# Kernel tuning notes

Measured on AMD Instinct MI355X. Metric: run time of the kernel, lower is better.

## Reference

```python
import jax, jax.numpy as jnp
import numpy as np

CAP = 15.0
EPS = 1e-6
NUM_HEADS = 16
HEAD_DIM = 64

def _rmsnorm(x, w):
    xf = x.astype(jnp.float32)
    var = jnp.mean(xf * xf, axis=-1, keepdims=True)
    return w * (xf * jax.lax.rsqrt(var + EPS)).astype(x.dtype)

def _gate(g):
    # sigmoid(soft_cap(g)) with cap 15
    return jax.nn.sigmoid(CAP * jnp.tanh(g / CAP))

def setup_inputs() -> dict:
    key = jax.random.key(0)
    ks = jax.random.split(key, 4)
    B, S, D = 4, 2048, 1024
    H, Dh = NUM_HEADS, HEAD_DIM
    return {
        "x": jax.random.normal(ks[0], (B, S, D), jnp.float32),
        "hidden_state": jnp.zeros((B, H, Dh, Dh), jnp.float32),
        "w_rms": jnp.ones((D,), jnp.float32),
        "w_qkv": jax.random.normal(ks[1], (D, 3 * H * Dh), jnp.float32) * 0.02,
        "w_gate": jax.random.normal(ks[2], (D, 3 * H), jnp.float32) * 0.02,
        "w_out": jax.random.normal(ks[3], (D, D), jnp.float32) * 0.02,
    }

def reference(x, hidden_state, w_rms, w_qkv, w_gate, w_out):
    B, S, D = x.shape
    H, Dh = NUM_HEADS, HEAD_DIM
    residual = x
    xn = _rmsnorm(x, w_rms)
    qkv = (xn @ w_qkv).reshape(B, S, 3, H, Dh)
    q, k, v = qkv[:, :, 0], qkv[:, :, 1], qkv[:, :, 2]  # [B,S,H,Dh]
    gates = _gate((xn @ w_gate).reshape(B, S, 3, H))
    i_g, f_g, o_g = gates[:, :, 0], gates[:, :, 1], gates[:, :, 2]  # [B,S,H]

    # time-major for scan: [S,B,H,...]
    def tm(a):
        return jnp.moveaxis(a, 1, 0)

    def step(state, inp):
        qt, kt, vt, it, ft, ot = inp  # [B,H,Dh]/[B,H]
        kv = kt[..., :, None] * vt[..., None, :]            # [B,H,Dh,Dh]
        state = ft[..., None, None] * state + it[..., None, None] * kv
        h = jnp.einsum('bhd,bhde->bhe', qt, state) * ot[..., None]
        return state, h

    _, h_seq = jax.lax.scan(step, hidden_state,
                            (tm(q), tm(k), tm(v), tm(i_g), tm(f_g), tm(o_g)))
    out = jnp.moveaxis(h_seq, 0, 1).reshape(B, S, H * Dh) @ w_out
    return residual + out
```

## Files before the change

kernel.cpp:

```cpp
#include <hip/hip_runtime.h>
#include <math.h>

typedef unsigned short u16;
typedef unsigned int   u32;
typedef __bf16 bf16x8 __attribute__((ext_vector_type(8)));
typedef float  f32x4  __attribute__((ext_vector_type(4)));

#define NBATCH 4
#define SEQ    2048
#define DIM    1024
#define NH     16
#define BH     64
#define NC     32
#define ROWS   8192
#define N1     3328

__device__ __forceinline__ u16 f2bf(float f) {
  u32 u = __builtin_bit_cast(u32, f);
  u32 r = u + 0x7fffu + ((u >> 16) & 1u);
  return (u16)(r >> 16);
}
__device__ __forceinline__ float bf2f(u16 h) {
  return __builtin_bit_cast(float, (u32)h << 16);
}

__device__ __forceinline__ void gl2lds16(const u16* g, u16* l) {
  __builtin_amdgcn_global_load_lds(
      (const __attribute__((address_space(1))) u32*)g,
      (__attribute__((address_space(3))) u32*)l, 16, 0, 0);
}

__global__ __launch_bounds__(256) void transpose_w(const float* __restrict__ W,
                                                   u16* __restrict__ Bt, int K, int N) {
  __shared__ float tile[32][33];
  const int n0 = blockIdx.x * 32, k0 = blockIdx.y * 32;
  const int tx = threadIdx.x, ty = threadIdx.y;
  #pragma unroll
  for (int i = 0; i < 4; i++)
    tile[ty + i * 8][tx] = W[(size_t)(k0 + ty + i * 8) * N + n0 + tx];
  __syncthreads();
  #pragma unroll
  for (int i = 0; i < 4; i++)
    Bt[(size_t)(n0 + ty + i * 8) * K + k0 + tx] = f2bf(tile[tx][ty + i * 8]);
}

__global__ __launch_bounds__(256) void fill_gateW(const float* __restrict__ wg,
                                                  u16* __restrict__ Bt) {
  const int g = blockIdx.x;
  const int tid = threadIdx.x;
  #pragma unroll
  for (int kk = 0; kk < 4; kk++) {
    const int k = kk * 256 + tid;
    u16 v = 0;
    if (g < 48) v = f2bf(wg[(size_t)k * 48 + g]);
    Bt[(size_t)(3072 + g) * 1024 + k] = v;
  }
}

__global__ __launch_bounds__(256) void rmsnorm_k(const float* __restrict__ x,
                                                 const float* __restrict__ w,
                                                 u16* __restrict__ xn) {
  const int row = blockIdx.x, tid = threadIdx.x;
  const float4 xv = *(const float4*)&x[(size_t)row * 1024 + tid * 4];
  float ss = xv.x * xv.x + xv.y * xv.y + xv.z * xv.z + xv.w * xv.w;
  #pragma unroll
  for (int off = 32; off > 0; off >>= 1) ss += __shfl_down(ss, off);
  __shared__ float red[4];
  if ((tid & 63) == 0) red[tid >> 6] = ss;
  __syncthreads();
  const float tot = red[0] + red[1] + red[2] + red[3];
  const float scale = rsqrtf(tot * (1.0f / 1024.0f) + 1e-6f);
  const float4 wv = *(const float4*)&w[tid * 4];
  const u16 o0 = f2bf(xv.x * scale * wv.x), o1 = f2bf(xv.y * scale * wv.y);
  const u16 o2 = f2bf(xv.z * scale * wv.z), o3 = f2bf(xv.w * scale * wv.w);
  uint2 ov;
  ov.x = (u32)o0 | ((u32)o1 << 16);
  ov.y = (u32)o2 | ((u32)o3 << 16);
  *(uint2*)&xn[(size_t)row * 1024 + tid * 4] = ov;
}


#define FENCE asm volatile("" ::: "memory")
#define SBAR  do { FENCE; __builtin_amdgcn_s_barrier(); FENCE; } while (0)
#define WAITV4 do { FENCE; asm volatile("s_waitcnt vmcnt(4)" ::: "memory"); } while (0)
#define WAITV0 do { FENCE; asm volatile("s_waitcnt vmcnt(0)" ::: "memory"); } while (0)

#define STAGE_A(BUF, HALF, TILE) do { \
  const u16* s_ = Abase + (size_t)(TILE) * 64 + (size_t)(HALF) * 131072; \
  u16* l_ = &lds[((BUF) * 4 + (HALF)) * 8192 + tid * 8]; \
  gl2lds16(s_, l_); gl2lds16(s_ + 65536, l_ + 4096); \
} while (0)

#define STAGE_B(BUF, HALF, TILE) do { \
  const u16* s_ = Bbase + (size_t)(TILE) * 64 + (size_t)(HALF) * 131072; \
  u16* l_ = &lds[((BUF) * 4 + 2 + (HALF)) * 8192 + tid * 8]; \
  gl2lds16(s_, l_); gl2lds16(s_ + 65536, l_ + 4096); \
} while (0)

#define READ_A(ALDS, MH) do { \
  _Pragma("unroll") \
  for (int mi_ = 0; mi_ < 4; ++mi_) { \
    af[mi_][0] = *(const bf16x8*)((ALDS) + (MH) * 4096 + mi_ * 1024 + co0); \
    af[mi_][1] = *(const bf16x8*)((ALDS) + (MH) * 4096 + mi_ * 1024 + co1); \
  } \
} while (0)

#define READ_B(BLDS, NH) do { \
  _Pragma("unroll") \
  for (int ni_ = 0; ni_ < 2; ++ni_) { \
    bfr[NH][ni_][0] = *(const bf16x8*)((BLDS) + (NH) * 2048 + ni_ * 1024 + co0); \
    bfr[NH][ni_][1] = *(const bf16x8*)((BLDS) + (NH) * 2048 + ni_ * 1024 + co1); \
  } \
} while (0)

#define MFMA16(MH, NH) do { \
  __builtin_amdgcn_s_setprio(1); \
  _Pragma("unroll") \
  for (int mi_ = 0; mi_ < 4; ++mi_) { \
    _Pragma("unroll") \
    for (int ni_ = 0; ni_ < 2; ++ni_) { \
      acc[(MH)*4+mi_][(NH)*2+ni_] = __builtin_amdgcn_mfma_f32_16x16x32_bf16( \
          af[mi_][0], bfr[NH][ni_][0], acc[(MH)*4+mi_][(NH)*2+ni_], 0, 0, 0); \
      acc[(MH)*4+mi_][(NH)*2+ni_] = __builtin_amdgcn_mfma_f32_16x16x32_bf16( \
          af[mi_][1], bfr[NH][ni_][1], acc[(MH)*4+mi_][(NH)*2+ni_], 0, 0, 0); \
    } \
  } \
  __builtin_amdgcn_s_setprio(0); \
} while (0)

#define GITER(T, FULL) do { \
   READ_A(aLds0, 0); READ_B(bLds0, 0); STAGE_A(1, 0, 2*(T)+1); \
         SBAR; MFMA16(0, 0); SBAR; \
   READ_B(bLds0, 1); STAGE_A(1, 1, 2*(T)+1); \
         SBAR; MFMA16(0, 1); SBAR; \
   READ_A(aLds0, 1); if (FULL) STAGE_B(0, 0, 2*(T)+2); \
         SBAR; MFMA16(1, 0); SBAR; \
   if (FULL) STAGE_B(0, 1, 2*(T)+2); \
         SBAR; MFMA16(1, 1); if (FULL) { WAITV4; } else { WAITV0; } SBAR; \
   READ_A(aLds1, 0); READ_B(bLds1, 0); if (FULL) STAGE_A(0, 0, 2*(T)+2); \
         SBAR; MFMA16(0, 0); SBAR; \
   READ_B(bLds1, 1); if (FULL) STAGE_A(0, 1, 2*(T)+2); \
         SBAR; MFMA16(0, 1); SBAR; \
   READ_A(aLds1, 1); if (FULL) STAGE_B(1, 0, 2*(T)+3); \
         SBAR; MFMA16(1, 0); SBAR; \
   if (FULL) STAGE_B(1, 1, 2*(T)+3); \
         SBAR; MFMA16(1, 1); if (FULL) { WAITV4; } SBAR; \
} while (0)

__global__ __launch_bounds__(512, 2) void gemm_qkv(const u16* __restrict__ A, const u16* __restrict__ Bt,
                                                   u16* __restrict__ Qb, u16* __restrict__ Kb,
                                                   u16* __restrict__ Vb, float* __restrict__ gates) {
  __shared__ __attribute__((aligned(16))) u16 lds[65536];
  const int tid = threadIdx.x;
  const int lane = tid & 63, wave = tid >> 6;
  const int q = lane >> 4, m16 = lane & 15;
  const int wm = wave & 1, wn = wave >> 1;

  const int g = blockIdx.x;
  const int swz = (g & 7) * 52 + (g >> 3);
  const int bm = swz & 31, bn = swz >> 5;
  const int rowBase = bm * 256, colBase = bn * 256;

  const int sx = m16 & 7;
  const int co0 = (q ^ sx) * 8;
  const int co1 = ((4 + q) ^ sx) * 8;

  const int r0 = tid >> 3, pc = tid & 7;
  const int lcg = pc ^ (r0 & 7);
  const u16* Abase = A  + (size_t)rowBase * 1024 + (size_t)r0 * 1024 + lcg * 8;
  const u16* Bbase = Bt + (size_t)colBase * 1024 + (size_t)r0 * 1024 + lcg * 8;

  const u16* aLds0 = &lds[wm * 8192 + m16 * 64];
  const u16* aLds1 = aLds0 + 32768;
  const u16* bLds0 = &lds[16384 + (wn >> 1) * 8192 + ((wn & 1) * 64 + m16) * 64];
  const u16* bLds1 = bLds0 + 32768;

  bf16x8 af[4][2];
  bf16x8 bfr[2][2][2];
  f32x4 acc[8][4] = {};

  STAGE_A(0, 0, 0); STAGE_A(0, 1, 0); STAGE_B(0, 0, 0); STAGE_B(0, 1, 0);
  STAGE_B(1, 0, 1); STAGE_B(1, 1, 1);
  WAITV4; SBAR;

  #pragma unroll 1
  for (int t = 0; t < 7; ++t) GITER(t, 1);
  GITER(7, 0);

  const int rr = lane >> 2, co = (lane & 3) * 16;
  if (colBase < 3072) {
    const int which = colBase >> 10;
    u16* dstBase = (which == 0) ? Qb : ((which == 1) ? Kb : Vb);
    const int b = rowBase >> 11;
    const int h = ((colBase & 1023) >> 6) + wn;
    const int tRow0 = (rowBase & 2047) + wm * 128;
    u16* headBase = dstBase + ((size_t)(b * 16 + h)) * 2048 * 64;
    u16* scratch = lds + wave * 1024;
    #pragma unroll
    for (int mi = 0; mi < 8; ++mi) {
      #pragma unroll
      for (int bj = 0; bj < 4; ++bj)
        #pragma unroll
        for (int r = 0; r < 4; ++r)
          scratch[(q * 4 + r) * 64 + bj * 16 + m16] = f2bf(acc[mi][bj][r]);
      const uint4 d0 = *(const uint4*)&scratch[rr * 64 + co];
      const uint4 d1 = *(const uint4*)&scratch[rr * 64 + co + 8];
      u16* gp = headBase + (size_t)(tRow0 + mi * 16 + rr) * 64 + co;
      *(uint4*)gp = d0;
      *(uint4*)(gp + 8) = d1;
    }
  } else {
    if (wn == 0) {
      #pragma unroll
      for (int ai = 0; ai < 8; ++ai)
        #pragma unroll
        for (int bj = 0; bj < 3; ++bj)
          #pragma unroll
          for (int r = 0; r < 4; ++r) {
            const int grow = rowBase + wm * 128 + ai * 16 + q * 4 + r;
            const int b = grow >> 11, tt = grow & 2047;
            const float v = acc[ai][bj][r];
            const float gg = 1.0f / (1.0f + expf(-(15.0f * tanhf(v * (1.0f / 15.0f)))));
            gates[((size_t)bj * 64 + (b * 16 + m16)) * 2048 + tt] = gg;
          }
    }
  }
}

__device__ __forceinline__ void gemm_core128(const u16* __restrict__ A, const u16* __restrict__ Bt,
                                             int K, int rowBase, int colBase,
                                             u16* As, u16* Bs, f32x4 (&acc)[4][4]) {
  const int tid = threadIdx.x;
  const int lane = tid & 63;
  const int q = lane >> 4, m16 = lane & 15;
  const int wave = tid >> 6;
  const int wm = wave & 1, wn = wave >> 1;
  const u16* gA[4]; u16* lA[4];
  const u16* gB[4]; u16* lB[4];
  #pragma unroll
  for (int j = 0; j < 4; j++) {
    const int c = tid + j * 256;
    const int half = c >> 9, cc = c & 511;
    gA[j] = &A [(size_t)(rowBase + (cc >> 2)) * K + half * 32 + (cc & 3) * 8];
    lA[j] = As + c * 8;
    gB[j] = &Bt[(size_t)(colBase + (cc >> 2)) * K + half * 32 + (cc & 3) * 8];
    lB[j] = Bs + c * 8;
  }
  for (int kb = 0; kb < K / 64; ++kb) {
    __syncthreads();
    #pragma unroll
    for (int j = 0; j < 4; j++) { gl2lds16(gA[j], lA[j]); gA[j] += 64; }
    #pragma unroll
    for (int j = 0; j < 4; j++) { gl2lds16(gB[j], lB[j]); gB[j] += 64; }
    __syncthreads();
    #pragma unroll
    for (int ks = 0; ks < 2; ks++) {
      const int off = ks * 4096;
      bf16x8 af[4], bfr[4];
      #pragma unroll
      for (int mi = 0; mi < 4; mi++)
        af[mi] = *(const bf16x8*)&As[off + (wm * 64 + mi * 16 + m16) * 32 + q * 8];
      #pragma unroll
      for (int ni = 0; ni < 4; ni++)
        bfr[ni] = *(const bf16x8*)&Bs[off + (wn * 64 + ni * 16 + m16) * 32 + q * 8];
      #pragma unroll
      for (int mi = 0; mi < 4; mi++)
        #pragma unroll
        for (int ni = 0; ni < 4; ni++)
          acc[mi][ni] = __builtin_amdgcn_mfma_f32_16x16x32_bf16(af[mi], bfr[ni], acc[mi][ni], 0, 0, 0);
    }
  }
}

__global__ __launch_bounds__(256, 4) void gemm_out(const u16* __restrict__ A, const u16* __restrict__ Bt,
                                                   const float* __restrict__ resid,
                                                   float* __restrict__ out) {
  __shared__ __attribute__((aligned(16))) u16 As[128 * 64];
  __shared__ __attribute__((aligned(16))) u16 Bs[128 * 64];
  f32x4 acc[4][4] = {};
  const int rowBase = blockIdx.x * 128, colBase = blockIdx.y * 128;
  gemm_core128(A, Bt, 1024, rowBase, colBase, As, Bs, acc);
  const int tid = threadIdx.x;
  const int lane = tid & 63, wave = tid >> 6;
  const int q = lane >> 4, m16 = lane & 15;
  const int wm = wave & 1, wn = wave >> 1;
  #pragma unroll
  for (int mi = 0; mi < 4; mi++)
    #pragma unroll
    for (int ni = 0; ni < 4; ni++)
      #pragma unroll
      for (int r = 0; r < 4; r++) {
        const int grow = rowBase + wm * 64 + mi * 16 + q * 4 + r;
        const int gcol = colBase + wn * 64 + ni * 16 + m16;
        const size_t idx = (size_t)grow * 1024 + gcol;
        out[idx] = acc[mi][ni][r] + resid[idx];
      }
}

__global__ __launch_bounds__(256) void passA_k(const u16* __restrict__ Qb, const u16* __restrict__ Kb,
                                               const u16* __restrict__ Vb,
                                               const float* __restrict__ gates,
                                               float* __restrict__ la,
                                               u16* __restrict__ Mbuf, u16* __restrict__ hseq) {
  __shared__ u16 Ql[64][72], Kl[64][72], KTl[64][72], VTl[64][72], Pl[64][72];
  __shared__ float laS[64], iS[64];
  const int tid = threadIdx.x;
  const int bh = blockIdx.x >> 5, c = blockIdx.x & 31;
  const int lane = tid & 63, w = tid >> 6;
  const int q = lane >> 4, m16 = lane & 15;
  const size_t base = ((size_t)bh * 2048 + c * 64) * 64;
  const int toff = c * 64;

  if (tid < 64) {
    float lg = logf(gates[(size_t)(64 + bh) * 2048 + toff + tid]);
    #pragma unroll
    for (int off = 1; off < 64; off <<= 1) {
      const float y = __shfl_up(lg, off);
      if (tid >= off) lg += y;
    }
    laS[tid] = lg;
    iS[tid] = gates[(size_t)bh * 2048 + toff + tid];
    la[(size_t)bh * 2048 + toff + tid] = lg;
  }
  __syncthreads();

  {
    const int s = tid >> 2, db = (tid & 3) * 16;
    const float wk = expf(laS[63] - laS[s]) * iS[s];
    const uint4 q0 = *(const uint4*)&Qb[base + s * 64 + db];
    const uint4 q1 = *(const uint4*)&Qb[base + s * 64 + db + 8];
    *(uint4*)&Ql[s][db] = q0;
    *(uint4*)&Ql[s][db + 8] = q1;
    const uint4 k0 = *(const uint4*)&Kb[base + s * 64 + db];
    const uint4 k1 = *(const uint4*)&Kb[base + s * 64 + db + 8];
    *(uint4*)&Kl[s][db] = k0;
    *(uint4*)&Kl[s][db + 8] = k1;
    u16 ktmp[16];
    *(uint4*)&ktmp[0] = k0;
    *(uint4*)&ktmp[8] = k1;
    #pragma unroll
    for (int j = 0; j < 16; j++) KTl[db + j][s] = f2bf(wk * bf2f(ktmp[j]));
    const uint4 v0 = *(const uint4*)&Vb[base + s * 64 + db];
    const uint4 v1 = *(const uint4*)&Vb[base + s * 64 + db + 8];
    u16 vtmp[16];
    *(uint4*)&vtmp[0] = v0;
    *(uint4*)&vtmp[8] = v1;
    #pragma unroll
    for (int j = 0; j < 16; j++) VTl[db + j][s] = vtmp[j];
  }
  __syncthreads();

  f32x4 pacc[4] = {};
  #pragma unroll
  for (int ks = 0; ks < 2; ks++) {
    const bf16x8 aq = *(const bf16x8*)&Ql[w * 16 + m16][ks * 32 + q * 8];
    #pragma unroll
    for (int ni = 0; ni < 4; ni++) {
      const bf16x8 bk = *(const bf16x8*)&Kl[ni * 16 + m16][ks * 32 + q * 8];
      pacc[ni] = __builtin_amdgcn_mfma_f32_16x16x32_bf16(aq, bk, pacc[ni], 0, 0, 0);
    }
  }
  #pragma unroll
  for (int ni = 0; ni < 4; ni++)
    #pragma unroll
    for (int r = 0; r < 4; r++) {
      const int tt = w * 16 + q * 4 + r, ss = ni * 16 + m16;
      float Wts = 0.0f;
      if (ss <= tt) Wts = expf(laS[tt] - laS[ss]) * iS[ss];
      Pl[tt][ss] = f2bf(pacc[ni][r] * Wts);
    }
  __syncthreads();

  f32x4 hacc[4] = {}, macc[4] = {};
  #pragma unroll
  for (int ks = 0; ks < 2; ks++) {
    const bf16x8 ap = *(const bf16x8*)&Pl[w * 16 + m16][ks * 32 + q * 8];
    const bf16x8 av = *(const bf16x8*)&VTl[w * 16 + m16][ks * 32 + q * 8];
    #pragma unroll
    for (int ni = 0; ni < 4; ni++) {
      const bf16x8 bv = *(const bf16x8*)&VTl[ni * 16 + m16][ks * 32 + q * 8];
      const bf16x8 bk = *(const bf16x8*)&KTl[ni * 16 + m16][ks * 32 + q * 8];
      hacc[ni] = __builtin_amdgcn_mfma_f32_16x16x32_bf16(ap, bv, hacc[ni], 0, 0, 0);
      macc[ni] = __builtin_amdgcn_mfma_f32_16x16x32_bf16(av, bk, macc[ni], 0, 0, 0);
    }
  }
  const int b = bh >> 4, h = bh & 15;
  #pragma unroll
  for (int ni = 0; ni < 4; ni++)
    #pragma unroll
    for (int r = 0; r < 4; r++) {
      const int tt = w * 16 + q * 4 + r, e = ni * 16 + m16;
      const int tg = c * 64 + tt;
      hseq[((size_t)b * 2048 + tg) * 1024 + h * 64 + e] = f2bf(hacc[ni][r]);
      Mbuf[(((size_t)bh * 32 + c) * 64 + tt) * 64 + e] = f2bf(macc[ni][r]);
    }
}

__global__ __launch_bounds__(256) void passB_k(u16* __restrict__ Mbuf,
                                               const float* __restrict__ hidden,
                                               const float* __restrict__ la) {
  const int bh = blockIdx.x >> 4;
  const int e = (blockIdx.x & 15) * 256 + threadIdx.x;
  __shared__ float Gs[32];
  if (threadIdx.x < 32)
    Gs[threadIdx.x] = expf(la[(size_t)bh * 2048 + threadIdx.x * 64 + 63]);
  __syncthreads();
  const int eRow = e >> 6, dCol = e & 63;
  float st = hidden[(size_t)bh * 4096 + dCol * 64 + eRow];
  u16* M = &Mbuf[(size_t)bh * 32 * 4096 + e];
  float m_next = bf2f(M[0]);
  #pragma unroll 4
  for (int c = 0; c < 32; c++) {
    const float m_cur = m_next;
    if (c < 31) m_next = bf2f(M[(size_t)(c + 1) * 4096]);
    M[(size_t)c * 4096] = f2bf(st);
    st = Gs[c] * st + m_cur;
  }
}

__global__ __launch_bounds__(256) void passC_k(const u16* __restrict__ Qb,
                                               const u16* __restrict__ SprevT,
                                               const float* __restrict__ la,
                                               const float* __restrict__ gates,
                                               u16* __restrict__ hseq) {
  __shared__ u16 aQl[64][72], STl[64][72];
  __shared__ float laS[64], oS[64];
  const int tid = threadIdx.x;
  const int bh = blockIdx.x >> 5, c = blockIdx.x & 31;
  const int lane = tid & 63, w = tid >> 6;
  const int q = lane >> 4, m16 = lane & 15;
  const size_t base = ((size_t)bh * 2048 + c * 64) * 64;
  const int toff = c * 64;
  if (tid < 64) {
    laS[tid] = la[(size_t)bh * 2048 + toff + tid];
    oS[tid] = gates[(size_t)(128 + bh) * 2048 + toff + tid];
  }
  {
    const int s = tid >> 2, db = (tid & 3) * 16;
    *(uint4*)&aQl[s][db]     = *(const uint4*)&Qb[base + s * 64 + db];
    *(uint4*)&aQl[s][db + 8] = *(const uint4*)&Qb[base + s * 64 + db + 8];
    const u16* SpT = &SprevT[((size_t)bh * 32 + c) * 4096];
    *(uint4*)&STl[s][db]     = *(const uint4*)&SpT[s * 64 + db];
    *(uint4*)&STl[s][db + 8] = *(const uint4*)&SpT[s * 64 + db + 8];
  }
  __syncthreads();
  f32x4 acc[4] = {};
  #pragma unroll
  for (int ks = 0; ks < 2; ks++) {
    const bf16x8 a = *(const bf16x8*)&aQl[w * 16 + m16][ks * 32 + q * 8];
    #pragma unroll
    for (int ni = 0; ni < 4; ni++) {
      const bf16x8 bb = *(const bf16x8*)&STl[ni * 16 + m16][ks * 32 + q * 8];
      acc[ni] = __builtin_amdgcn_mfma_f32_16x16x32_bf16(a, bb, acc[ni], 0, 0, 0);
    }
  }
  const int b = bh >> 4, h = bh & 15;
  #pragma unroll
  for (int ni = 0; ni < 4; ni++)
    #pragma unroll
    for (int r = 0; r < 4; r++) {
      const int tt = w * 16 + q * 4 + r, e = ni * 16 + m16;
      const int tg = c * 64 + tt;
      const float a_t = expf(laS[tt]);
      const float o = oS[tt];
      const size_t idx = ((size_t)b * 2048 + tg) * 1024 + h * 64 + e;
      hseq[idx] = f2bf(o * (bf2f(hseq[idx]) + a_t * acc[ni][r]));
    }
}

extern "C" void kernel_launch(void* const* d_in, const int* in_sizes, int n_in,
                              void* d_out, int out_size, void* d_ws, size_t ws_size,
                              hipStream_t stream) {
  (void)in_sizes; (void)n_in; (void)out_size; (void)ws_size;
  const float* x      = (const float*)d_in[0];
  const float* hidden = (const float*)d_in[1];
  const float* w_rms  = (const float*)d_in[2];
  const float* w_qkv  = (const float*)d_in[3];
  const float* w_gate = (const float*)d_in[4];
  const float* w_out  = (const float*)d_in[5];
  float* out = (float*)d_out;

  char* p = (char*)d_ws;
  u16* wqkvT = (u16*)p;  p += (size_t)N1 * 1024 * 2;
  u16* woutT = (u16*)p;  p += (size_t)1024 * 1024 * 2;
  u16* xn    = (u16*)p;  p += (size_t)ROWS * 1024 * 2;
  u16* Qb    = (u16*)p;  p += (size_t)BH * 2048 * 64 * 2;
  u16* Kb    = (u16*)p;  p += (size_t)BH * 2048 * 64 * 2;
  u16* Vb    = (u16*)p;  p += (size_t)BH * 2048 * 64 * 2;
  float* gates = (float*)p; p += (size_t)3 * BH * 2048 * 4;
  float* la    = (float*)p; p += (size_t)BH * 2048 * 4;
  u16* Mbuf  = (u16*)p;  p += (size_t)BH * NC * 4096 * 2;
  u16* hseq  = (u16*)p;  p += (size_t)ROWS * 1024 * 2;

  transpose_w<<<dim3(96, 32), dim3(32, 8), 0, stream>>>(w_qkv, wqkvT, 1024, 3072);
  transpose_w<<<dim3(32, 32), dim3(32, 8), 0, stream>>>(w_out, woutT, 1024, 1024);
  fill_gateW<<<256, 256, 0, stream>>>(w_gate, wqkvT);
  rmsnorm_k<<<ROWS, 256, 0, stream>>>(x, w_rms, xn);
  gemm_qkv<<<416, 512, 0, stream>>>(xn, wqkvT, Qb, Kb, Vb, gates);
  passA_k<<<BH * NC, 256, 0, stream>>>(Qb, Kb, Vb, gates, la, Mbuf, hseq);
  passB_k<<<BH * 16, 256, 0, stream>>>(Mbuf, hidden, la);
  passC_k<<<BH * NC, 256, 0, stream>>>(Qb, Mbuf, la, gates, hseq);
  gemm_out<<<dim3(64, 8), 256, 0, stream>>>(hseq, woutT, x, out);
}
```

Baseline: 264.1 us.

## Reuse pipelined 256x256 GEMM core for output projection and reorder QKV tiles

Factors the software-pipelined, swizzled-LDS 256x256 GEMM core of the QKV projection into shared macros and uses it for the output projection. This replaces the simple 128x128 kernel that synced twice per k-step. The output GEMM now launches 128 blocks of 512 threads with a swizzled tile order. Fewer, larger blocks may leave half the CUs idle, while each tile gets more reuse and better load/compute overlap. The QKV GEMM tile mapping also changes from column-major to row-major over the 32x13 tile grid, which changes L2 reuse.

```diff
diff --git a/kernel.cpp b/kernel.cpp
--- a/kernel.cpp
+++ b/kernel.cpp
@@ -147,45 +147,47 @@
          SBAR; MFMA16(1, 1); if (FULL) { WAITV4; } SBAR; \
 } while (0)
 
+#define CORE_SETUP(AROWBASE, BCOLBASE) \
+  const int tid = threadIdx.x; \
+  const int lane = tid & 63, wave = tid >> 6; \
+  const int q = lane >> 4, m16 = lane & 15; \
+  const int wm = wave & 1, wn = wave >> 1; \
+  const int sx = m16 & 7; \
+  const int co0 = (q ^ sx) * 8; \
+  const int co1 = ((4 + q) ^ sx) * 8; \
+  const int r0 = tid >> 3, pc = tid & 7; \
+  const int lcg = pc ^ (r0 & 7); \
+  const u16* Abase = (AROWBASE) + (size_t)r0 * 1024 + lcg * 8; \
+  const u16* Bbase = (BCOLBASE) + (size_t)r0 * 1024 + lcg * 8; \
+  const u16* aLds0 = &lds[wm * 8192 + m16 * 64]; \
+  const u16* aLds1 = aLds0 + 32768; \
+  const u16* bLds0 = &lds[16384 + (wn >> 1) * 8192 + ((wn & 1) * 64 + m16) * 64]; \
+  const u16* bLds1 = bLds0 + 32768; \
+  bf16x8 af[4][2]; \
+  bf16x8 bfr[2][2][2]; \
+  f32x4 acc[8][4] = {};
+
+#define CORE_RUN16() do { \
+  STAGE_A(0, 0, 0); STAGE_A(0, 1, 0); STAGE_B(0, 0, 0); STAGE_B(0, 1, 0); \
+  STAGE_B(1, 0, 1); STAGE_B(1, 1, 1); \
+  WAITV4; SBAR; \
+  _Pragma("unroll 1") \
+  for (int t = 0; t < 7; ++t) GITER(t, 1); \
+  GITER(7, 0); \
+} while (0)
+
 __global__ __launch_bounds__(512, 2) void gemm_qkv(const u16* __restrict__ A, const u16* __restrict__ Bt,
                                                    u16* __restrict__ Qb, u16* __restrict__ Kb,
                                                    u16* __restrict__ Vb, float* __restrict__ gates) {
   __shared__ __attribute__((aligned(16))) u16 lds[65536];
-  const int tid = threadIdx.x;
-  const int lane = tid & 63, wave = tid >> 6;
-  const int q = lane >> 4, m16 = lane & 15;
-  const int wm = wave & 1, wn = wave >> 1;
 
   const int g = blockIdx.x;
   const int swz = (g & 7) * 52 + (g >> 3);
-  const int bm = swz & 31, bn = swz >> 5;
+  const int bm = swz / 13, bn = swz % 13;
   const int rowBase = bm * 256, colBase = bn * 256;
 
-  const int sx = m16 & 7;
-  const int co0 = (q ^ sx) * 8;
-  const int co1 = ((4 + q) ^ sx) * 8;
-
-  const int r0 = tid >> 3, pc = tid & 7;
-  const int lcg = pc ^ (r0 & 7);
-  const u16* Abase = A  + (size_t)rowBase * 1024 + (size_t)r0 * 1024 + lcg * 8;
-  const u16* Bbase = Bt + (size_t)colBase * 1024 + (size_t)r0 * 1024 + lcg * 8;
-
-  const u16* aLds0 = &lds[wm * 8192 + m16 * 64];
-  const u16* aLds1 = aLds0 + 32768;
-  const u16* bLds0 = &lds[16384 + (wn >> 1) * 8192 + ((wn & 1) * 64 + m16) * 64];
-  const u16* bLds1 = bLds0 + 32768;
-
-  bf16x8 af[4][2];
-  bf16x8 bfr[2][2][2];
-  f32x4 acc[8][4] = {};
-
-  STAGE_A(0, 0, 0); STAGE_A(0, 1, 0); STAGE_B(0, 0, 0); STAGE_B(0, 1, 0);
-  STAGE_B(1, 0, 1); STAGE_B(1, 1, 1);
-  WAITV4; SBAR;
-
-  #pragma unroll 1
-  for (int t = 0; t < 7; ++t) GITER(t, 1);
-  GITER(7, 0);
+  CORE_SETUP(A + (size_t)rowBase * 1024, Bt + (size_t)colBase * 1024);
+  CORE_RUN16();
 
   const int rr = lane >> 2, co = (lane & 3) * 16;
   if (colBase < 3072) {
@@ -227,73 +229,30 @@
   }
 }
 
-__device__ __forceinline__ void gemm_core128(const u16* __restrict__ A, const u16* __restrict__ Bt,
-                                             int K, int rowBase, int colBase,
-                                             u16* As, u16* Bs, f32x4 (&acc)[4][4]) {
-  const int tid = threadIdx.x;
-  const int lane = tid & 63;
-  const int q = lane >> 4, m16 = lane & 15;
-  const int wave = tid >> 6;
-  const int wm = wave & 1, wn = wave >> 1;
-  const u16* gA[4]; u16* lA[4];
-  const u16* gB[4]; u16* lB[4];
-  #pragma unroll
-  for (int j = 0; j < 4; j++) {
-    const int c = tid + j * 256;
-    const int half = c >> 9, cc = c & 511;
-    gA[j] = &A [(size_t)(rowBase + (cc >> 2)) * K + half * 32 + (cc & 3) * 8];
-    lA[j] = As + c * 8;
-    gB[j] = &Bt[(size_t)(colBase + (cc >> 2)) * K + half * 32 + (cc & 3) * 8];
-    lB[j] = Bs + c * 8;
-  }
-  for (int kb = 0; kb < K / 64; ++kb) {
-    __syncthreads();
-    #pragma unroll
-    for (int j = 0; j < 4; j++) { gl2lds16(gA[j], lA[j]); gA[j] += 64; }
-    #pragma unroll
-    for (int j = 0; j < 4; j++) { gl2lds16(gB[j], lB[j]); gB[j] += 64; }
-    __syncthreads();
-    #pragma unroll
-    for (int ks = 0; ks < 2; ks++) {
-      const int off = ks * 4096;
-      bf16x8 af[4], bfr[4];
-      #pragma unroll
-      for (int mi = 0; mi < 4; mi++)
-        af[mi] = *(const bf16x8*)&As[off + (wm * 64 + mi * 16 + m16) * 32 + q * 8];
-      #pragma unroll
-      for (int ni = 0; ni < 4; ni++)
-        bfr[ni] = *(const bf16x8*)&Bs[off + (wn * 64 + ni * 16 + m16) * 32 + q * 8];
-      #pragma unroll
-      for (int mi = 0; mi < 4; mi++)
-        #pragma unroll
-        for (int ni = 0; ni < 4; ni++)
-          acc[mi][ni] = __builtin_amdgcn_mfma_f32_16x16x32_bf16(af[mi], bfr[ni], acc[mi][ni], 0, 0, 0);
-    }
-  }
-}
-
-__global__ __launch_bounds__(256, 4) void gemm_out(const u16* __restrict__ A, const u16* __restrict__ Bt,
+__global__ __launch_bounds__(512, 2) void gemm_out(const u16* __restrict__ A, const u16* __restrict__ Bt,
                                                    const float* __restrict__ resid,
                                                    float* __restrict__ out) {
-  __shared__ __attribute__((aligned(16))) u16 As[128 * 64];
-  __shared__ __attribute__((aligned(16))) u16 Bs[128 * 64];
-  f32x4 acc[4][4] = {};
-  const int rowBase = blockIdx.x * 128, colBase = blockIdx.y * 128;
-  gemm_core128(A, Bt, 1024, rowBase, colBase, As, Bs, acc);
-  const int tid = threadIdx.x;
-  const int lane = tid & 63, wave = tid >> 6;
-  const int q = lane >> 4, m16 = lane & 15;
-  const int wm = wave & 1, wn = wave >> 1;
-  #pragma unroll
-  for (int mi = 0; mi < 4; mi++)
-    #pragma unroll
-    for (int ni = 0; ni < 4; ni++)
+  __shared__ __attribute__((aligned(16))) u16 lds[65536];
+
+  const int g = blockIdx.x;
+  const int swz = (g & 7) * 16 + (g >> 3);
+  const int bm = swz >> 2, bn = swz & 3;
+  const int rowBase = bm * 256, colBase = bn * 256;
+
+  CORE_SETUP(A + (size_t)rowBase * 1024, Bt + (size_t)colBase * 1024);
+  CORE_RUN16();
+
+  const int colW = colBase + (wn >> 1) * 128 + (wn & 1) * 64;
+  #pragma unroll
+  for (int mi = 0; mi < 8; ++mi)
+    #pragma unroll
+    for (int bj = 0; bj < 4; ++bj)
       #pragma unroll
-      for (int r = 0; r < 4; r++) {
-        const int grow = rowBase + wm * 64 + mi * 16 + q * 4 + r;
-        const int gcol = colBase + wn * 64 + ni * 16 + m16;
+      for (int r = 0; r < 4; ++r) {
+        const int grow = rowBase + wm * 128 + mi * 16 + q * 4 + r;
+        const int gcol = colW + bj * 16 + m16;
         const size_t idx = (size_t)grow * 1024 + gcol;
-        out[idx] = acc[mi][ni][r] + resid[idx];
+        out[idx] = acc[mi][bj][r] + resid[idx];
       }
 }
 
@@ -500,5 +459,5 @@
   passA_k<<<BH * NC, 256, 0, stream>>>(Qb, Kb, Vb, gates, la, Mbuf, hseq);
   passB_k<<<BH * 16, 256, 0, stream>>>(Mbuf, hidden, la);
   passC_k<<<BH * NC, 256, 0, stream>>>(Qb, Mbuf, la, gates, hseq);
-  gemm_out<<<dim3(64, 8), 256, 0, stream>>>(hseq, woutT, x, out);
-}
+  gemm_out<<<128, 512, 0, stream>>>(hseq, woutT, x, out);
+}
```

New measurement: 258.6 us. -2.1%, faster.
